# Performance work log

Measured on AMD Instinct MI355X. Metric: run time of the kernel, lower is better.

The kernel has to match this reference:

```python
import jax, jax.numpy as jnp
import numpy as np

# Block sizes (DGL message-flow-graph / sampled blocks)
NS0, ND0, NE0 = 300000, 50000, 800000   # block0: 2-hop frontier -> 1-hop frontier
NS1, ND1, NE1 = 50000, 8192, 131072     # block1: 1-hop frontier -> seed nodes


def _graph_conv(x, src, dst, ew, W, b, n_src, n_dst, weight_first):
    """DGL GraphConv with norm='both' and edge_weight.

    x: [n_src, d_in] source-node features; (src, dst): edge endpoints;
    ew: [E] edge weights. Degrees are UNWEIGHTED (copy of DGL semantics),
    clamped to >= 1. Weight applied before aggregation iff d_in > d_out.
    """
    ones_e = jnp.ones_like(ew)
    out_deg = jnp.clip(jax.ops.segment_sum(ones_e, src, num_segments=n_src), 1.0, None)
    h = x * (out_deg ** -0.5)[:, None]
    if weight_first:
        h = h @ W
    # gather-weight-scatter: m_v = sum_{e: e->v} ew_e * h_{src_e}
    msg = jax.ops.segment_sum(ew[:, None] * h[src], dst, num_segments=n_dst)
    in_deg = jnp.clip(jax.ops.segment_sum(ones_e, dst, num_segments=n_dst), 1.0, None)
    msg = msg * (in_deg ** -0.5)[:, None]
    if not weight_first:
        msg = msg @ W
    return msg + b


def setup_inputs() -> dict:
    key = jax.random.key(0)
    ks = jax.random.split(key, 12)
    in_f, hid_f, out_f = 256, 128, 128
    return {
        "x": jax.random.normal(ks[0], (NS0, in_f), dtype=jnp.float32),
        "src0": jax.random.randint(ks[1], (NE0,), 0, NS0, dtype=jnp.int64 if jax.config.jax_enable_x64 else jnp.int32).astype(jnp.int32),
        "dst0": jax.random.randint(ks[2], (NE0,), 0, ND0).astype(jnp.int32),
        "ew0": jax.random.normal(ks[3], (NE0,), dtype=jnp.float32),
        "src1": jax.random.randint(ks[4], (NE1,), 0, NS1).astype(jnp.int32),
        "dst1": jax.random.randint(ks[5], (NE1,), 0, ND1).astype(jnp.int32),
        "ew1": jax.random.normal(ks[6], (NE1,), dtype=jnp.float32),
        "W1": jax.random.normal(ks[7], (in_f, hid_f), dtype=jnp.float32) * 0.05,
        "b1": jax.random.normal(ks[8], (hid_f,), dtype=jnp.float32) * 0.05,
        "W2": jax.random.normal(ks[9], (hid_f, out_f), dtype=jnp.float32) * 0.05,
        "b2": jax.random.normal(ks[10], (out_f,), dtype=jnp.float32) * 0.05,
    }


def reference(x, src0, dst0, ew0, src1, dst1, ew1, W1, b1, W2, b2):
    # layer 1: in(256) > hidden(128) -> weight applied before aggregation
    h = jax.nn.relu(_graph_conv(x, src0, dst0, ew0, W1, b1, NS0, ND0, weight_first=True))
    # layer 2: hidden(128) <= out(128) -> aggregate then weight
    out = jax.nn.relu(_graph_conv(h, src1, dst1, ew1, W2, b2, NS1, ND1, weight_first=False))
    return out  # [ND1, out_f]
```

## Files before the change

### kernel.cpp

```cpp
#include <hip/hip_runtime.h>

#define NS0 300000
#define ND0 50000
#define NE0 800000
#define NS1 50000
#define ND1 8192
#define NE1 131072
#define IN_F 256
#define HID_F 128
#define SLOTS 64
#define NTILE (NS0 / 16)
#define GEMM_GRID 2048
#define BUILD_GRID 512

typedef __attribute__((ext_vector_type(8))) _Float16 half8_t;
typedef __attribute__((ext_vector_type(4))) _Float16 half4_t;
typedef __attribute__((ext_vector_type(4))) float f32x4;

#define OFF_OUTDEG0I 0
#define OFF_OUTDEG1I 300000
#define OFF_CNT0     350000
#define OFF_CNT1     400000
#define ZERO_WORDS   408192
#define OFF_EDGE0    408192
#define OFF_EDGE1    6808192
#define OFF_H1       7856768
#define OFF_W1T      14256768
#define OFF_G        14273152

__global__ __launch_bounds__(256) void k_init(
    int4* __restrict__ p, const float* __restrict__ W1,
    _Float16* __restrict__ w1t) {
  if (blockIdx.x < 128) {
    int i = blockIdx.x * 256 + threadIdx.x;
    for (; i < ZERO_WORDS / 4; i += 128 * 256) p[i] = make_int4(0, 0, 0, 0);
  } else {
    int i = (blockIdx.x - 128) * 256 + threadIdx.x;
    for (; i < IN_F * HID_F; i += 32 * 256) {
      int k = i >> 7, n = i & 127;
      w1t[n * 256 + k] = (_Float16)W1[i];
    }
  }
}

#define LDB(p, o) (*reinterpret_cast<const half8_t*>((p) + (o)))
__global__ __launch_bounds__(256) void k_gemm_build(
    const float* __restrict__ x, const _Float16* __restrict__ w1t,
    _Float16* __restrict__ g,
    const int* __restrict__ src0, const int* __restrict__ dst0,
    const float* __restrict__ ew0, int* __restrict__ outdeg0,
    int* __restrict__ cnt0, int2* __restrict__ edge0,
    const int* __restrict__ src1, const int* __restrict__ dst1,
    const float* __restrict__ ew1, int* __restrict__ outdeg1,
    int* __restrict__ cnt1, int2* __restrict__ edge1) {
  __shared__ __align__(16) _Float16 ldsA[2][16 * 256];
  __shared__ _Float16 ldsT[4][16 * 40];

  if (blockIdx.x < BUILD_GRID) {
    int tid = blockIdx.x * 256 + threadIdx.x;
    int stride = BUILD_GRID * 256;
    for (int i = tid; i < NE0; i += stride) {
      int s = src0[i];
      int d = dst0[i];
      float w = ew0[i];
      atomicAdd(&outdeg0[s], 1);
      int slot = atomicAdd(&cnt0[d], 1);
      if (slot < SLOTS) edge0[d * SLOTS + slot] = make_int2(s, __float_as_int(w));
    }
    for (int i = tid; i < NE1; i += stride) {
      int s = src1[i];
      int d = dst1[i];
      float w = ew1[i];
      atomicAdd(&outdeg1[s], 1);
      int slot = atomicAdd(&cnt1[d], 1);
      if (slot < SLOTS) edge1[d * SLOTS + slot] = make_int2(s, __float_as_int(w));
    }
    return;
  }

  const int tid = threadIdx.x;
  const int wv = tid >> 6;
  const int lane = tid & 63;
  const int m = lane & 15;
  const int grp = lane >> 4;
  _Float16* tp = ldsT[wv];

  const _Float16* wb0 = w1t + (size_t)(32 * wv + m) * 256 + grp * 8;
  const _Float16* wb1 = wb0 + 16 * 256;
  const half8_t b00 = LDB(wb0, 0),   b01 = LDB(wb0, 32),  b02 = LDB(wb0, 64),
                b03 = LDB(wb0, 96),  b04 = LDB(wb0, 128), b05 = LDB(wb0, 160),
                b06 = LDB(wb0, 192), b07 = LDB(wb0, 224);
  const half8_t b10 = LDB(wb1, 0),   b11 = LDB(wb1, 32),  b12 = LDB(wb1, 64),
                b13 = LDB(wb1, 96),  b14 = LDB(wb1, 128), b15 = LDB(wb1, 160),
                b16 = LDB(wb1, 192), b17 = LDB(wb1, 224);

  const int skb = lane >> 3;
  const int sgrp = (lane >> 1) & 3;
  const int sjh = lane & 1;
  const int row_r = lane >> 2;
  const int q_r   = lane & 3;

  const int bid = blockIdx.x - BUILD_GRID;
  float4 pv1[4], pv2[4];

#define LOAD_PV(PV, T)                                                         \
  {                                                                            \
    const float* tb = x + (size_t)(T) * 4096;                                  \
    _Pragma("unroll") for (int r = 0; r < 4; ++r)                              \
        PV[r] = *reinterpret_cast<const float4*>(tb + tid * 4 + r * 1024);     \
  }

#define WRITE_LDS(BUFI, PV)                                                    \
  {                                                                            \
    char* Bp = reinterpret_cast<char*>(&ldsA[BUFI][0]);                        \
    _Pragma("unroll") for (int r = 0; r < 4; ++r) {                            \
      const int mr = wv + 4 * r;                                               \
      half4_t h;                                                               \
      h[0] = (_Float16)PV[r].x; h[1] = (_Float16)PV[r].y;                      \
      h[2] = (_Float16)PV[r].z; h[3] = (_Float16)PV[r].w;                      \
      const int idx = skb * 64 + sgrp * 16 + mr;                               \
      const int S = idx ^ skb ^ sgrp;                                          \
      *reinterpret_cast<half4_t*>(Bp + S * 16 + sjh * 8) = h;                  \
    }                                                                          \
  }

#define STEP(A, KB, B0, B1)                                                    \
  {                                                                            \
    const int Sr = ((KB * 64 + lane) ^ KB ^ grp);                              \
    const half8_t af = *reinterpret_cast<const half8_t*>(A + Sr * 16);         \
    acc0 = __builtin_amdgcn_mfma_f32_16x16x32_f16(af, B0, acc0, 0, 0, 0);      \
    acc1 = __builtin_amdgcn_mfma_f32_16x16x32_f16(af, B1, acc1, 0, 0, 0);      \
  }

#define COMPUTE_TILE(BUFI, T)                                                  \
  {                                                                            \
    const char* A = reinterpret_cast<const char*>(&ldsA[BUFI][0]);             \
    f32x4 acc0 = {0.f, 0.f, 0.f, 0.f};                                         \
    f32x4 acc1 = {0.f, 0.f, 0.f, 0.f};                                         \
    STEP(A, 0, b00, b10) STEP(A, 1, b01, b11)                                  \
    STEP(A, 2, b02, b12) STEP(A, 3, b03, b13)                                  \
    STEP(A, 4, b04, b14) STEP(A, 5, b05, b15)                                  \
    STEP(A, 6, b06, b16) STEP(A, 7, b07, b17)                                  \
    _Pragma("unroll") for (int r = 0; r < 4; ++r) {                            \
      tp[(4 * grp + r) * 40 + m]      = (_Float16)acc0[r];                     \
      tp[(4 * grp + r) * 40 + 16 + m] = (_Float16)acc1[r];                     \
    }                                                                          \
    const half8_t ov =                                                         \
        *reinterpret_cast<const half8_t*>(tp + row_r * 40 + q_r * 8);          \
    *reinterpret_cast<half8_t*>(                                               \
        g + (size_t)((T) * 16 + row_r) * 128 + 32 * wv + q_r * 8) = ov;        \
  }

  {
    const float* tb = x + (size_t)bid * 4096;
#pragma unroll
    for (int r = 0; r < 4; ++r) {
      const int mr = wv + 4 * r;
      const float4 v = *reinterpret_cast<const float4*>(tb + tid * 4 + r * 1024);
      half4_t h;
      h[0] = (_Float16)v.x; h[1] = (_Float16)v.y;
      h[2] = (_Float16)v.z; h[3] = (_Float16)v.w;
      const int idx = skb * 64 + sgrp * 16 + mr;
      const int S = idx ^ skb ^ sgrp;
      *reinterpret_cast<half4_t*>(
          reinterpret_cast<char*>(&ldsA[0][0]) + S * 16 + sjh * 8) = h;
    }
  }
  if (bid + GEMM_GRID < NTILE) LOAD_PV(pv1, bid + GEMM_GRID);
  __syncthreads();

  for (int t = bid; t < NTILE; t += 2 * GEMM_GRID) {
    const int tA2 = t + 2 * GEMM_GRID;
    if (tA2 < NTILE) LOAD_PV(pv2, tA2);
    COMPUTE_TILE(0, t);
    if (t + GEMM_GRID < NTILE) WRITE_LDS(1, pv1);
    __syncthreads();
    const int tB = t + GEMM_GRID;
    if (tB < NTILE) {
      const int tB3 = t + 3 * GEMM_GRID;
      if (tB3 < NTILE) LOAD_PV(pv1, tB3);
      COMPUTE_TILE(1, tB);
      if (tA2 < NTILE) WRITE_LDS(0, pv2);
      __syncthreads();
    }
  }
#undef LOAD_PV
#undef WRITE_LDS
#undef STEP
#undef COMPUTE_TILE
}

__global__ __launch_bounds__(256) void k_gather1(
    const _Float16* __restrict__ g, const int* __restrict__ cnt,
    const int2* __restrict__ edge, const int* __restrict__ outdeg0,
    const int* __restrict__ outdeg1, const float* __restrict__ b1,
    float* __restrict__ h1) {
  const int w = (blockIdx.x * 256 + threadIdx.x) >> 6;
  const int lane = threadIdx.x & 63;
  const int gp = lane >> 4;
  const int sl = lane & 15;
  if (w >= ND0) return;
  const int deg = min(cnt[w], SLOTS);
  const int2* ep = edge + (size_t)w * SLOTS;
  float acc[8] = {0.f, 0.f, 0.f, 0.f, 0.f, 0.f, 0.f, 0.f};
  for (int e = 0; e < deg; e += 4) {
    const int idx = e + gp;
    int2 p = make_int2(0, 0);
    float c = 0.f;
    if (idx < deg) {
      p = ep[idx];
      c = __int_as_float(p.y) * rsqrtf(fmaxf((float)outdeg0[p.x], 1.0f));
    }
    const half8_t v =
        *reinterpret_cast<const half8_t*>(g + (size_t)p.x * 128 + sl * 8);
#pragma unroll
    for (int j = 0; j < 8; ++j) acc[j] = fmaf(c, (float)v[j], acc[j]);
  }
#pragma unroll
  for (int j = 0; j < 8; ++j) {
    acc[j] += __shfl_xor(acc[j], 16, 64);
    acc[j] += __shfl_xor(acc[j], 32, 64);
  }
  if (gp == 0) {
    const float sc = rsqrtf(fmaxf((float)deg, 1.0f));
    const float s1 = rsqrtf(fmaxf((float)outdeg1[w], 1.0f));
    const float4 bv0 = *reinterpret_cast<const float4*>(b1 + sl * 8);
    const float4 bv1 = *reinterpret_cast<const float4*>(b1 + sl * 8 + 4);
    float4 o0, o1;
    o0.x = fmaxf(fmaf(acc[0], sc, bv0.x), 0.0f) * s1;
    o0.y = fmaxf(fmaf(acc[1], sc, bv0.y), 0.0f) * s1;
    o0.z = fmaxf(fmaf(acc[2], sc, bv0.z), 0.0f) * s1;
    o0.w = fmaxf(fmaf(acc[3], sc, bv0.w), 0.0f) * s1;
    o1.x = fmaxf(fmaf(acc[4], sc, bv1.x), 0.0f) * s1;
    o1.y = fmaxf(fmaf(acc[5], sc, bv1.y), 0.0f) * s1;
    o1.z = fmaxf(fmaf(acc[6], sc, bv1.z), 0.0f) * s1;
    o1.w = fmaxf(fmaf(acc[7], sc, bv1.w), 0.0f) * s1;
    float* hr = h1 + (size_t)w * 128 + sl * 8;
    *reinterpret_cast<float4*>(hr) = o0;
    *reinterpret_cast<float4*>(hr + 4) = o1;
  }
}

#define FMA2(acc, c, v)        \
  acc.x = fmaf(c, v.x, acc.x); \
  acc.y = fmaf(c, v.y, acc.y);

__global__ __launch_bounds__(256) void k_layer2(
    const float* __restrict__ h1, const int* __restrict__ cnt,
    const int2* __restrict__ edge, const float* __restrict__ W2,
    const float* __restrict__ b2, float* __restrict__ out) {
  __shared__ float arow[8][HID_F];
  const int t = blockIdx.x;
  const int wv = threadIdx.x >> 6;
  const int lane = threadIdx.x & 63;

#pragma unroll
  for (int rr = 0; rr < 2; ++rr) {
    const int row = t * 8 + wv * 2 + rr;
    const int deg = min(cnt[row], SLOTS);
    const int2* ep = edge + (size_t)row * SLOTS;
    float2 acc = make_float2(0.f, 0.f);
    int e = 0;
    for (; e + 4 <= deg; e += 4) {
      int4 q0 = *reinterpret_cast<const int4*>(ep + e);
      int4 q1 = *reinterpret_cast<const int4*>(ep + e + 2);
      float2 v0 = *reinterpret_cast<const float2*>(h1 + (size_t)q0.x * HID_F + lane * 2);
      float2 v1 = *reinterpret_cast<const float2*>(h1 + (size_t)q0.z * HID_F + lane * 2);
      float2 v2 = *reinterpret_cast<const float2*>(h1 + (size_t)q1.x * HID_F + lane * 2);
      float2 v3 = *reinterpret_cast<const float2*>(h1 + (size_t)q1.z * HID_F + lane * 2);
      FMA2(acc, __int_as_float(q0.y), v0);
      FMA2(acc, __int_as_float(q0.w), v1);
      FMA2(acc, __int_as_float(q1.y), v2);
      FMA2(acc, __int_as_float(q1.w), v3);
    }
    for (; e < deg; ++e) {
      int2 p = ep[e];
      float2 v = *reinterpret_cast<const float2*>(h1 + (size_t)p.x * HID_F + lane * 2);
      FMA2(acc, __int_as_float(p.y), v);
    }
    const float sc = rsqrtf(fmaxf((float)deg, 1.0f));
    *reinterpret_cast<float2*>(&arow[wv * 2 + rr][lane * 2]) =
        make_float2(acc.x * sc, acc.y * sc);
  }
  __syncthreads();

  const int j = threadIdx.x & 127;
  const int rg = threadIdx.x >> 7;
  float a0 = 0.f, a1 = 0.f, a2 = 0.f, a3 = 0.f;
  const float* wj = W2 + j;
#pragma unroll 8
  for (int k = 0; k < HID_F; ++k) {
    const float wvv = wj[(size_t)k * 128];
    a0 = fmaf(arow[rg * 4 + 0][k], wvv, a0);
    a1 = fmaf(arow[rg * 4 + 1][k], wvv, a1);
    a2 = fmaf(arow[rg * 4 + 2][k], wvv, a2);
    a3 = fmaf(arow[rg * 4 + 3][k], wvv, a3);
  }
  const float bj = b2[j];
  const int row0 = t * 8 + rg * 4;
  out[(size_t)(row0 + 0) * 128 + j] = fmaxf(a0 + bj, 0.0f);
  out[(size_t)(row0 + 1) * 128 + j] = fmaxf(a1 + bj, 0.0f);
  out[(size_t)(row0 + 2) * 128 + j] = fmaxf(a2 + bj, 0.0f);
  out[(size_t)(row0 + 3) * 128 + j] = fmaxf(a3 + bj, 0.0f);
}

extern "C" void kernel_launch(void* const* d_in, const int* in_sizes, int n_in,
                              void* d_out, int out_size, void* d_ws, size_t ws_size,
                              hipStream_t stream) {
  const float* x    = (const float*)d_in[0];
  const int*   src0 = (const int*)d_in[1];
  const int*   dst0 = (const int*)d_in[2];
  const float* ew0  = (const float*)d_in[3];
  const int*   src1 = (const int*)d_in[4];
  const int*   dst1 = (const int*)d_in[5];
  const float* ew1  = (const float*)d_in[6];
  const float* W1   = (const float*)d_in[7];
  const float* b1   = (const float*)d_in[8];
  const float* W2   = (const float*)d_in[9];
  const float* b2   = (const float*)d_in[10];
  float* out = (float*)d_out;

  int*   wsi = (int*)d_ws;
  float* wsf = (float*)d_ws;
  int* outdeg0 = wsi + OFF_OUTDEG0I;
  int* outdeg1 = wsi + OFF_OUTDEG1I;
  int* cnt0    = wsi + OFF_CNT0;
  int* cnt1    = wsi + OFF_CNT1;
  int2* edge0  = (int2*)(wsi + OFF_EDGE0);
  int2* edge1  = (int2*)(wsi + OFF_EDGE1);
  float* h1    = wsf + OFF_H1;
  _Float16* w1t = (_Float16*)(wsi + OFF_W1T);
  _Float16* g   = (_Float16*)(wsi + OFF_G);

  k_init<<<160, 256, 0, stream>>>((int4*)d_ws, W1, w1t);
  k_gemm_build<<<GEMM_GRID + BUILD_GRID, 256, 0, stream>>>(
      x, w1t, g, src0, dst0, ew0, outdeg0, cnt0, edge0,
      src1, dst1, ew1, outdeg1, cnt1, edge1);
  k_gather1<<<(ND0 * 64) / 256, 256, 0, stream>>>(g, cnt0, edge0, outdeg0,
                                                  outdeg1, b1, h1);
  k_layer2<<<ND1 / 8, 256, 0, stream>>>(h1, cnt1, edge1, W2, b2, out);
}
```

Baseline: 229.8 us.

## Defer G tile stores through block-wide LDS buffer and halve GEMM grid

Result: no change. 233.8 us (+1.7%).

```diff
diff --git a/kernel.cpp b/kernel.cpp
--- a/kernel.cpp
+++ b/kernel.cpp
@@ -10,7 +10,7 @@
 #define HID_F 128
 #define SLOTS 64
 #define NTILE (NS0 / 16)
-#define GEMM_GRID 2048
+#define GEMM_GRID 1024
 #define BUILD_GRID 512
 
 typedef __attribute__((ext_vector_type(8))) _Float16 half8_t;
@@ -54,7 +54,7 @@
     const float* __restrict__ ew1, int* __restrict__ outdeg1,
     int* __restrict__ cnt1, int2* __restrict__ edge1) {
   __shared__ __align__(16) _Float16 ldsA[2][16 * 256];
-  __shared__ _Float16 ldsT[4][16 * 40];
+  __shared__ __align__(16) _Float16 outT[2][16 * 128];
 
   if (blockIdx.x < BUILD_GRID) {
     int tid = blockIdx.x * 256 + threadIdx.x;
@@ -83,7 +83,6 @@
   const int lane = tid & 63;
   const int m = lane & 15;
   const int grp = lane >> 4;
-  _Float16* tp = ldsT[wv];
 
   const _Float16* wb0 = w1t + (size_t)(32 * wv + m) * 256 + grp * 8;
   const _Float16* wb1 = wb0 + 16 * 256;
@@ -97,11 +96,15 @@
   const int skb = lane >> 3;
   const int sgrp = (lane >> 1) & 3;
   const int sjh = lane & 1;
-  const int row_r = lane >> 2;
-  const int q_r   = lane & 3;
 
   const int bid = blockIdx.x - BUILD_GRID;
   float4 pv1[4], pv2[4];
+
+#define BARRIER()                                                              \
+  __builtin_amdgcn_sched_barrier(0);                                           \
+  asm volatile("s_waitcnt lgkmcnt(0)");                                        \
+  __builtin_amdgcn_s_barrier();                                                \
+  __builtin_amdgcn_sched_barrier(0);
 
 #define LOAD_PV(PV, T)                                                         \
   {                                                                            \
@@ -132,7 +135,7 @@
     acc1 = __builtin_amdgcn_mfma_f32_16x16x32_f16(af, B1, acc1, 0, 0, 0);      \
   }
 
-#define COMPUTE_TILE(BUFI, T)                                                  \
+#define COMPUTE_TILE(BUFI)                                                     \
   {                                                                            \
     const char* A = reinterpret_cast<const char*>(&ldsA[BUFI][0]);             \
     f32x4 acc0 = {0.f, 0.f, 0.f, 0.f};                                         \
@@ -142,13 +145,17 @@
     STEP(A, 4, b04, b14) STEP(A, 5, b05, b15)                                  \
     STEP(A, 6, b06, b16) STEP(A, 7, b07, b17)                                  \
     _Pragma("unroll") for (int r = 0; r < 4; ++r) {                            \
-      tp[(4 * grp + r) * 40 + m]      = (_Float16)acc0[r];                     \
-      tp[(4 * grp + r) * 40 + 16 + m] = (_Float16)acc1[r];                     \
+      outT[BUFI][(4 * grp + r) * 128 + 32 * wv + m]      = (_Float16)acc0[r];  \
+      outT[BUFI][(4 * grp + r) * 128 + 32 * wv + 16 + m] = (_Float16)acc1[r];  \
     }                                                                          \
-    const half8_t ov =                                                         \
-        *reinterpret_cast<const half8_t*>(tp + row_r * 40 + q_r * 8);          \
+  }
+
+#define STORE_G(T, BUFI)                                                       \
+  {                                                                            \
+    const half8_t ov = *reinterpret_cast<const half8_t*>(                      \
+        &outT[BUFI][(tid >> 4) * 128 + (tid & 15) * 8]);                       \
     *reinterpret_cast<half8_t*>(                                               \
-        g + (size_t)((T) * 16 + row_r) * 128 + 32 * wv + q_r * 8) = ov;        \
+        g + ((size_t)(T) * 16 + (tid >> 4)) * 128 + (tid & 15) * 8) = ov;      \
   }
 
   {
@@ -167,27 +174,41 @@
     }
   }
   if (bid + GEMM_GRID < NTILE) LOAD_PV(pv1, bid + GEMM_GRID);
-  __syncthreads();
-
+  BARRIER();
+
+  int lastT = -1, lastB = 0;
   for (int t = bid; t < NTILE; t += 2 * GEMM_GRID) {
+    if (lastT >= 0) STORE_G(lastT, 1);
     const int tA2 = t + 2 * GEMM_GRID;
     if (tA2 < NTILE) LOAD_PV(pv2, tA2);
-    COMPUTE_TILE(0, t);
+    COMPUTE_TILE(0);
     if (t + GEMM_GRID < NTILE) WRITE_LDS(1, pv1);
-    __syncthreads();
+    BARRIER();
+    lastT = t; lastB = 0;
     const int tB = t + GEMM_GRID;
     if (tB < NTILE) {
+      STORE_G(lastT, 0);
       const int tB3 = t + 3 * GEMM_GRID;
       if (tB3 < NTILE) LOAD_PV(pv1, tB3);
-      COMPUTE_TILE(1, tB);
+      COMPUTE_TILE(1);
       if (tA2 < NTILE) WRITE_LDS(0, pv2);
-      __syncthreads();
-    }
-  }
+      BARRIER();
+      lastT = tB; lastB = 1;
+    }
+  }
+  if (lastT >= 0) {
+    if (lastB == 0) {
+      STORE_G(lastT, 0);
+    } else {
+      STORE_G(lastT, 1);
+    }
+  }
+#undef BARRIER
 #undef LOAD_PV
 #undef WRITE_LDS
 #undef STEP
 #undef COMPUTE_TILE
+#undef STORE_G
 }
 
 __global__ __launch_bounds__(256) void k_gather1(
```
